# Kernel optimization log

Measured on AMD Instinct MI355X. Metric: run time of the kernel, lower is better.

Reference implementation:

```python
import jax, jax.numpy as jnp
import numpy as np

L = 2          # n layers
P = 768        # input_p_dim
Q = 768        # input_q_dim
H = 768        # hidden (nhids[i])
A = 768        # attention dim
B, T, TQ = 16, 128, 128
EPS = 1e-6


def setup_inputs() -> dict:
    key = jax.random.key(0)
    ks = jax.random.split(key, 12)
    stdv = 1.0 / np.sqrt(H)
    u = lambda k, shp: jax.random.uniform(k, shp, jnp.float32, -stdv, stdv)
    return {
        "input_p": jax.random.normal(ks[0], (B, T, P), jnp.float32),
        "mask_p": jnp.ones((B, T), jnp.float32),
        "input_q": jax.random.normal(ks[1], (B, TQ, Q), jnp.float32),
        "mask_q": jnp.ones((B, TQ), jnp.float32),
        # LSTMCell params (stacked over layers; input size = in_d + Q = P + Q)
        "W_ih": u(ks[2], (L, P + Q, 4 * H)),
        "W_hh": u(ks[3], (L, H, 4 * H)),
        "bias": jnp.zeros((L, 4 * H), jnp.float32),
        # LayerNorm params (gamma=1, beta=0 as in reset_parameters-style init)
        "ln_i_gamma": jnp.ones((L, 4 * H), jnp.float32),
        "ln_i_beta": jnp.zeros((L, 4 * H), jnp.float32),
        "ln_h_gamma": jnp.ones((L, 4 * H), jnp.float32),
        "ln_h_beta": jnp.zeros((L, 4 * H), jnp.float32),
        "ln_c_gamma": jnp.ones((L, H), jnp.float32),
        "ln_c_beta": jnp.zeros((L, H), jnp.float32),
        # match-attention params
        "Wq": u(ks[4], (L, Q, A)),
        "Wp": u(ks[5], (L, P, A)),   # in_d == P == H for both layers
        "Wr": u(ks[6], (L, H, A)),
        "w_att": u(ks[7], (L, A)),
        "b_att": u(ks[8], (L, A)),
    }


def _layernorm(x, gamma, beta, mask):
    # Faithful to the repo's LayerNorm: mean over last dim, var over dim=1
    # (identical for 2D x), unbiased variance (torch default), eps added twice.
    mean = x.mean(-1, keepdims=True)
    var = x.var(-1, ddof=1, keepdims=True)
    out = gamma * (x - mean) / (jnp.sqrt(var + EPS) + EPS) + beta
    return out * mask[:, None]


def reference(input_p, mask_p, input_q, mask_q, W_ih, W_hh, bias,
              ln_i_gamma, ln_i_beta, ln_h_gamma, ln_h_beta,
              ln_c_gamma, ln_c_beta, Wq, Wp, Wr, w_att, b_att):
    nlayers, hid = W_hh.shape[0], W_hh.shape[1]
    bsz, tlen, _ = input_p.shape
    # q @ Wq is time-invariant: hoist out of the recurrence. (L, B, Tq, A)
    qWq = jnp.einsum("bsd,lda->lbsa", input_q, Wq)

    def step(carry, xs):
        h, c = carry                      # each (L, B, H)
        p_t, m_t = xs                     # (B, P), (B,)
        m = m_t[:, None]
        cur = p_t
        hs, cs = [], []
        for d in range(nlayers):
            # --- match attention over q, conditioned on (cur, h_tm1) ---
            s = cur @ Wp[d] + h[d] @ Wr[d] + b_att[d]          # (B, A)
            G = jnp.tanh(qWq[d] + s[:, None, :])               # (B, Tq, A)
            scores = G @ w_att[d]                              # (B, Tq)
            scores = jnp.where(mask_q > 0, scores, -1e9)
            alpha = jax.nn.softmax(scores, axis=-1)
            weighted = jnp.einsum("bs,bsd->bd", alpha, input_q)
            x = jnp.concatenate([cur, weighted], axis=-1)      # (B, in_d + Q)
            # --- LSTM cell with inline layernorm + masking ---
            wi = _layernorm(x @ W_ih[d], ln_i_gamma[d], ln_i_beta[d], m_t)
            wh = _layernorm(h[d] @ W_hh[d], ln_h_gamma[d], ln_h_beta[d], m_t)
            pre = wi + wh + bias[d]
            f, i, o, g = jnp.split(pre, 4, axis=-1)            # order: f,i,o,g
            c1 = jax.nn.sigmoid(f) * c[d] + jax.nn.sigmoid(i) * jnp.tanh(g)
            c1 = c1 * m + c[d] * (1.0 - m)
            h1 = jax.nn.sigmoid(o) * jnp.tanh(
                _layernorm(c1, ln_c_gamma[d], ln_c_beta[d], m_t))
            h1 = h1 * m + h[d] * (1.0 - m)
            hs.append(h1)
            cs.append(c1)
            cur = h1
        return (jnp.stack(hs), jnp.stack(cs)), cur             # emit top-layer h

    h0 = jnp.zeros((nlayers, bsz, hid), input_p.dtype)
    c0 = jnp.zeros_like(h0)
    xs = (jnp.transpose(input_p, (1, 0, 2)), jnp.transpose(mask_p, (1, 0)))
    _, ys = jax.lax.scan(step, (h0, c0), xs)                   # ys: (T, B, H)
    states = jnp.transpose(ys, (1, 0, 2))                      # (B, T, H)
    return (states, mask_p)
```

## Files before the change

kernel.cpp:

```cpp
#include <hip/hip_runtime.h>
#include <math.h>

#define NBLK 512
#define NTHR 256

typedef float f32x4 __attribute__((ext_vector_type(4)));

__device__ __forceinline__ float2 ld2a(const float* p){
    unsigned long long u = __hip_atomic_load((const unsigned long long*)p,
                                             __ATOMIC_RELAXED, __HIP_MEMORY_SCOPE_AGENT);
    float2 r;
    r.x = __uint_as_float((unsigned)u);
    r.y = __uint_as_float((unsigned)(u >> 32));
    return r;
}
__device__ __forceinline__ void st2a(float* p, float a, float b){
    unsigned long long u = (unsigned long long)__float_as_uint(a)
                         | ((unsigned long long)__float_as_uint(b) << 32);
    __hip_atomic_store((unsigned long long*)p, u,
                       __ATOMIC_RELAXED, __HIP_MEMORY_SCOPE_AGENT);
}
__device__ __forceinline__ float ld1a(const float* p){
    unsigned u = __hip_atomic_load((const unsigned*)p, __ATOMIC_RELAXED, __HIP_MEMORY_SCOPE_AGENT);
    return __uint_as_float(u);
}
__device__ __forceinline__ void st1a(float* p, float v){
    __hip_atomic_store((unsigned*)p, __float_as_uint(v), __ATOMIC_RELAXED, __HIP_MEMORY_SCOPE_AGENT);
}

__device__ __forceinline__ float fsigmoid(float x){ return 1.0f/(1.0f + __expf(-x)); }
__device__ __forceinline__ float ftanh(float x){
    float e = __expf(2.0f*x);
    return 1.0f - 2.0f/(e + 1.0f);
}
__device__ __forceinline__ float dot4(f32x4 a, f32x4 b){
    return a.x*b.x + a.y*b.y + a.z*b.z + a.w*b.w;
}

struct Params {
    const float* input_p; const float* mask_p; const float* input_q; const float* mask_q;
    const float* W_ih; const float* W_hh; const float* bias;
    const float* ln_i_g; const float* ln_i_b; const float* ln_h_g; const float* ln_h_b;
    const float* ln_c_g; const float* ln_c_b;
    const float* Wq; const float* Wp; const float* Wr; const float* w_att; const float* b_att;
    float* out;
    float* qWq;
    float* iqT;
    float* pWp0;
    float* pWih0;
    float* h;
    float* c;
    float* sP;
    float* whP;
    float* cwP;
    float* wiP;
    float* wghtd;
    float* escore;
    unsigned* bar;
};

__device__ __forceinline__ void gsync(unsigned* bar, int bid, unsigned n){
    __syncthreads();
    if (threadIdx.x == 0){
        unsigned* leaf = bar + 128 + (bid >> 4)*32;
        unsigned old = __hip_atomic_fetch_add(leaf, 1u, __ATOMIC_RELAXED, __HIP_MEMORY_SCOPE_AGENT);
        if ((old & 15u) == 15u){
            unsigned rold = __hip_atomic_fetch_add(bar + 32, 1u, __ATOMIC_RELAXED, __HIP_MEMORY_SCOPE_AGENT);
            if ((rold & 31u) == 31u){
                __hip_atomic_store(bar, n + 1u, __ATOMIC_RELEASE, __HIP_MEMORY_SCOPE_AGENT);
            }
        }
        int spins = 0;
        while (__hip_atomic_load(bar, __ATOMIC_RELAXED, __HIP_MEMORY_SCOPE_AGENT) < n + 1u){
            __builtin_amdgcn_s_sleep(4);
            if (++spins > 1024){
                (void)__hip_atomic_load(bar, __ATOMIC_ACQUIRE, __HIP_MEMORY_SCOPE_AGENT);
                spins = 0;
            }
        }
    }
    __syncthreads();
}

__device__ __forceinline__ void stageA(
    const float* Aptr, int ars, int aco, int k0, bool coh, float* Ash, int tid)
{
    #pragma unroll
    for (int rep = 0; rep < 6; rep++){
        int i2 = tid + rep*256;
        int r = i2 / 96, kk = (i2 % 96)*2;
        const float* src = Aptr + (size_t)r*ars + aco + k0 + kk;
        float2 v;
        if (coh) v = ld2a(src); else v = *(const float2*)src;
        Ash[r*192 + kk]     = v.x;
        Ash[r*192 + kk + 1] = v.y;
    }
    __syncthreads();
}

__device__ __forceinline__ void mm192f(
    const float* W, int N, float* outP, int cbase, int k0,
    const float* Ash, int tid)
{
    int cg = tid & 15, rg = tid >> 4;
    int col = cbase + cg*4;
    const float* Wc = W + (size_t)k0*N + col;
    const float* Arow = Ash + rg*192;
    f32x4 acc = {0,0,0,0};
    f32x4 wA[8], wB[8];
    #pragma unroll
    for (int j = 0; j < 8; j++) wA[j] = *(const f32x4*)(Wc + (size_t)j*N);
    for (int kb = 0; kb < 192; kb += 16){
        #pragma unroll
        for (int j = 0; j < 8; j++) wB[j] = *(const f32x4*)(Wc + (size_t)(kb+8+j)*N);
        #pragma unroll
        for (int j = 0; j < 8; j++) acc += Arow[kb+j]*wA[j];
        if (kb < 176){
            #pragma unroll
            for (int j = 0; j < 8; j++) wA[j] = *(const f32x4*)(Wc + (size_t)(kb+16+j)*N);
        }
        #pragma unroll
        for (int j = 0; j < 8; j++) acc += Arow[kb+8+j]*wB[j];
    }
    float* o = outP + (size_t)rg*N + col;
    st2a(o,   acc.x, acc.y);
    st2a(o+2, acc.z, acc.w);
}

__device__ __forceinline__ float bsum4(float v, float* red, int tid){
    #pragma unroll
    for (int off = 32; off; off >>= 1) v += __shfl_xor(v, off);
    __syncthreads();
    if ((tid & 63) == 0) red[tid >> 6] = v;
    __syncthreads();
    float s = red[0]+red[1]+red[2]+red[3];
    __syncthreads();
    return s;
}

__global__ __launch_bounds__(NTHR, 2) void coop_kernel(Params p)
{
    __shared__ float smem[6936];
    const int tid = threadIdx.x;
    const int bid = blockIdx.x;
    unsigned n = 0;

    {
        int gid = bid*NTHR + tid;
        if (gid < 24576) st2a(p.h + gid*2, 0.f, 0.f);
        if (gid < 2048)  p.out[(size_t)16*128*768 + gid] = p.mask_p[gid];
    }
    gsync(p.bar, bid, n); n++;

    for (int t = 0; t < 128; ++t){
        for (int d = 0; d < 2; ++d){
            const float* h_d = p.h + (size_t)d*12288;

            {
                int ntile = (d == 0) ? 60 : 120;
                if (bid < ntile*4){
                    int tile = bid >> 2, kc = bid & 3, k0 = kc*192;
                    if (d == 0){
                        stageA(h_d, 768, 0, k0, true, smem, tid);
                        if (tile < 12){
                            mm192f(p.Wr, 768, p.sP + (size_t)kc*12288, tile*64, k0, smem, tid);
                        } else {
                            mm192f(p.W_hh, 3072, p.whP + (size_t)kc*49152, (tile-12)*64, k0, smem, tid);
                        }
                    } else {
                        bool useCur = (tile >= 12 && tile < 24) || (tile >= 72);
                        stageA(useCur ? p.h : h_d, 768, 0, k0, true, smem, tid);
                        if (tile < 12){
                            mm192f(p.Wr + (size_t)589824, 768,
                                   p.sP + (size_t)kc*12288, tile*64, k0, smem, tid);
                        } else if (tile < 24){
                            mm192f(p.Wp + (size_t)589824, 768,
                                   p.sP + (size_t)(4+kc)*12288, (tile-12)*64, k0, smem, tid);
                        } else if (tile < 72){
                            mm192f(p.W_hh + (size_t)2359296, 3072,
                                   p.whP + (size_t)kc*49152, (tile-24)*64, k0, smem, tid);
                        } else {
                            mm192f(p.W_ih + (size_t)4718592, 3072,
                                   p.cwP + (size_t)kc*49152, (tile-72)*64, k0, smem, tid);
                        }
                    }
                }
            }
            gsync(p.bar, bid, n); n++;

            if (bid < 256){
                int b = bid >> 4, sq0 = (bid & 15)*8;
                float* s_sh  = smem;
                float* wa_sh = smem + 768;
                if (tid < 192){
                    f32x4 acc = *(const f32x4*)(p.b_att + d*768 + tid*4);
                    if (d == 0){
                        f32x4 pv = *(const f32x4*)(p.pWp0 + ((size_t)b*128 + t)*768 + tid*4);
                        acc += pv;
                    }
                    int ncp = (d == 0) ? 4 : 8;
                    for (int cp = 0; cp < ncp; cp++){
                        const float* src = p.sP + (size_t)cp*12288 + b*768 + tid*4;
                        float2 u0 = ld2a(src);
                        float2 u1 = ld2a(src + 2);
                        acc.x += u0.x; acc.y += u0.y; acc.z += u1.x; acc.w += u1.y;
                    }
                    *(f32x4*)&s_sh[tid*4] = acc;
                } else {
                    int i0 = tid - 192;
                    for (int r = 0; r < 3; r++){
                        int i = i0 + r*64;
                        *(f32x4*)&wa_sh[i*4] = *(const f32x4*)(p.w_att + d*768 + i*4);
                    }
                }
                __syncthreads();
                int sq = sq0 + (tid >> 5), l = tid & 31;
                const float* qrow = p.qWq + ((size_t)(d*2048 + b*128 + sq))*768;
                float part = 0.f;
                #pragma unroll
                for (int i = 0; i < 6; i++){
                    int a = i*128 + l*4;
                    f32x4 q  = *(const f32x4*)(qrow + a);
                    f32x4 s4 = *(const f32x4*)(s_sh + a);
                    f32x4 w4 = *(const f32x4*)(wa_sh + a);
                    part += ftanh(q.x + s4.x)*w4.x + ftanh(q.y + s4.y)*w4.y
                          + ftanh(q.z + s4.z)*w4.z + ftanh(q.w + s4.w)*w4.w;
                }
                #pragma unroll
                for (int off = 16; off; off >>= 1) part += __shfl_xor(part, off, 32);
                if (l == 0){
                    float e = (p.mask_q[b*128 + sq] > 0.f) ? __expf(part) : 0.f;
                    st1a(p.escore + b*128 + sq, e);
                }
            }
            gsync(p.bar, bid, n); n++;

            if (bid < 64){
                int b = bid >> 2, cg = bid & 3;
                float* e_sh = smem;
                if (tid < 128) e_sh[tid] = ld1a(p.escore + b*128 + tid);
                __syncthreads();
                if (tid < 64){
                    float v = e_sh[tid] + e_sh[tid + 64];
                    #pragma unroll
                    for (int off = 32; off; off >>= 1) v += __shfl_xor(v, off);
                    if (tid == 0) e_sh[128] = 1.0f / v;
                }
                __syncthreads();
                float inv = e_sh[128];
                if (tid < 192){
                    int cc = cg*192 + tid;
                    const float* ip = p.iqT + ((size_t)b*768 + cc)*128;
                    float acc = 0.f;
                    #pragma unroll 8
                    for (int j = 0; j < 32; j++){
                        f32x4 q  = *(const f32x4*)(ip + j*4);
                        f32x4 e4 = *(const f32x4*)&e_sh[j*4];
                        acc += dot4(q, e4);
                    }
                    st1a(p.wghtd + b*768 + cc, acc*inv);
                }
            }
            gsync(p.bar, bid, n); n++;

            if (bid < 192){
                int tile = bid >> 2, kc = bid & 3, k0 = kc*192;
                stageA(p.wghtd, 768, 0, k0, true, smem, tid);
                mm192f(p.W_ih + (size_t)d*4718592 + (size_t)768*3072, 3072,
                       p.wiP + (size_t)kc*49152, tile*64, k0, smem, tid);
            }
            gsync(p.bar, bid, n); n++;

            if (bid < 16){
                const int b = bid;
                float* wi_sh = smem;
                float* wh_sh = smem + 3072;
                float* c_sh  = smem + 6144;
                float* red   = smem + 6928;
                const float mm = p.mask_p[b*128 + t];
                const float* gi = p.ln_i_g + d*3072; const float* bi = p.ln_i_b + d*3072;
                const float* gh = p.ln_h_g + d*3072; const float* bh = p.ln_h_b + d*3072;
                const float* gc = p.ln_c_g + d*768;  const float* bc = p.ln_c_b + d*768;
                const float* bias_d = p.bias + d*3072;

                float swi=0,qwi=0,swh=0,qwh=0;
                #pragma unroll
                for (int rep = 0; rep < 3; rep++){
                    int j4 = tid + rep*256;
                    int base = b*3072 + j4*4;
                    f32x4 a = {0,0,0,0};
                    f32x4 hvec = {0,0,0,0};
                    #pragma unroll
                    for (int cp = 0; cp < 4; cp++){
                        const float* s0 = p.wiP + (size_t)cp*49152 + base;
                        float2 u0 = ld2a(s0);
                        float2 u1 = ld2a(s0 + 2);
                        a.x += u0.x; a.y += u0.y; a.z += u1.x; a.w += u1.y;
                        const float* s1 = p.whP + (size_t)cp*49152 + base;
                        float2 v0 = ld2a(s1);
                        float2 v1 = ld2a(s1 + 2);
                        hvec.x += v0.x; hvec.y += v0.y; hvec.z += v1.x; hvec.w += v1.y;
                    }
                    if (d == 0){
                        f32x4 pv = *(const f32x4*)(p.pWih0 + ((size_t)b*128 + t)*3072 + j4*4);
                        a += pv;
                    } else {
                        #pragma unroll
                        for (int cp = 0; cp < 4; cp++){
                            const float* s2 = p.cwP + (size_t)cp*49152 + base;
                            float2 w0 = ld2a(s2);
                            float2 w1 = ld2a(s2 + 2);
                            a.x += w0.x; a.y += w0.y; a.z += w1.x; a.w += w1.y;
                        }
                    }
                    *(f32x4*)&wi_sh[j4*4] = a;
                    *(f32x4*)&wh_sh[j4*4] = hvec;
                    swi += a.x+a.y+a.z+a.w;
                    qwi += dot4(a,a);
                    swh += hvec.x+hvec.y+hvec.z+hvec.w;
                    qwh += dot4(hvec,hvec);
                }
                swi = bsum4(swi, red, tid);
                qwi = bsum4(qwi, red, tid);
                swh = bsum4(swh, red, tid);
                qwh = bsum4(qwh, red, tid);
                float mi = swi/3072.f, vi = fmaxf((qwi - 3072.f*mi*mi)/3071.f, 0.f);
                float mh = swh/3072.f, vh = fmaxf((qwh - 3072.f*mh*mh)/3071.f, 0.f);
                float ivi = 1.f/(sqrtf(vi + 1e-6f) + 1e-6f);
                float ivh = 1.f/(sqrtf(vh + 1e-6f) + 1e-6f);

                for (int j = tid; j < 3072; j += NTHR){
                    float pre = mm*(gi[j]*(wi_sh[j]-mi)*ivi + bi[j])
                              + mm*(gh[j]*(wh_sh[j]-mh)*ivh + bh[j])
                              + bias_d[j];
                    wi_sh[j] = pre;
                }
                __syncthreads();

                float sc=0,qc=0;
                for (int idx = tid; idx < 384; idx += NTHR){
                    int u = idx*2;
                    float2 c_old = ld2a(p.c + (size_t)d*12288 + b*768 + u);
                    float f0  = wi_sh[u],        f1  = wi_sh[u+1];
                    float i0  = wi_sh[768+u],    i1  = wi_sh[768+u+1];
                    float g0  = wi_sh[2304+u],   g1  = wi_sh[2304+u+1];
                    float c10 = fsigmoid(f0)*c_old.x + fsigmoid(i0)*ftanh(g0);
                    float c11 = fsigmoid(f1)*c_old.y + fsigmoid(i1)*ftanh(g1);
                    c10 = c10*mm + c_old.x*(1.f - mm);
                    c11 = c11*mm + c_old.y*(1.f - mm);
                    st2a(p.c + (size_t)d*12288 + b*768 + u, c10, c11);
                    c_sh[u] = c10; c_sh[u+1] = c11;
                    sc += c10 + c11; qc += c10*c10 + c11*c11;
                }
                sc = bsum4(sc, red, tid);
                qc = bsum4(qc, red, tid);
                float mc = sc/768.f, vc = fmaxf((qc - 768.f*mc*mc)/767.f, 0.f);
                float ivc = 1.f/(sqrtf(vc + 1e-6f) + 1e-6f);

                for (int idx = tid; idx < 384; idx += NTHR){
                    int u = idx*2;
                    float2 h_old = ld2a(p.h + (size_t)d*12288 + b*768 + u);
                    float o0 = wi_sh[1536+u], o1 = wi_sh[1536+u+1];
                    float l0 = (gc[u]*(c_sh[u]-mc)*ivc + bc[u])*mm;
                    float l1 = (gc[u+1]*(c_sh[u+1]-mc)*ivc + bc[u+1])*mm;
                    float h10 = fsigmoid(o0)*ftanh(l0);
                    float h11 = fsigmoid(o1)*ftanh(l1);
                    h10 = h10*mm + h_old.x*(1.f - mm);
                    h11 = h11*mm + h_old.y*(1.f - mm);
                    st2a(p.h + (size_t)d*12288 + b*768 + u, h10, h11);
                    if (d == 1){
                        float2 ov = { h10, h11 };
                        *(float2*)(p.out + ((size_t)b*128 + t)*768 + u) = ov;
                    }
                }
            }
            gsync(p.bar, bid, n); n++;
        }
    }
}

__global__ __launch_bounds__(256) void k_mm_pre(
    const float* __restrict__ Ain, const float* __restrict__ W,
    float* __restrict__ C, int ldw, int ncols)
{
    __shared__ float Ash[16][772];
    int rowbase = blockIdx.y*16;
    for (int r = 0; r < 16; r++)
        for (int i = threadIdx.x; i < 768; i += 256)
            Ash[r][i] = Ain[(size_t)(rowbase + r)*768 + i];
    __syncthreads();
    int lane = threadIdx.x & 63;
    int colq = lane & 15, rsub = lane >> 4, wq = threadIdx.x >> 6;
    int r = wq*4 + rsub;
    int col = blockIdx.x*64 + colq*4;
    float4 acc = {0.f,0.f,0.f,0.f};
    const float* Wc = W + col;
    for (int k = 0; k < 768; k += 4){
        float4 a4 = *(const float4*)&Ash[r][k];
        float4 w0 = *(const float4*)(Wc + (size_t)(k+0)*ldw);
        float4 w1 = *(const float4*)(Wc + (size_t)(k+1)*ldw);
        float4 w2 = *(const float4*)(Wc + (size_t)(k+2)*ldw);
        float4 w3 = *(const float4*)(Wc + (size_t)(k+3)*ldw);
        acc.x += a4.x*w0.x + a4.y*w1.x + a4.z*w2.x + a4.w*w3.x;
        acc.y += a4.x*w0.y + a4.y*w1.y + a4.z*w2.y + a4.w*w3.y;
        acc.z += a4.x*w0.z + a4.y*w1.z + a4.z*w2.z + a4.w*w3.z;
        acc.w += a4.x*w0.w + a4.y*w1.w + a4.z*w2.w + a4.w*w3.w;
    }
    *(float4*)(C + (size_t)(rowbase + r)*ncols + col) = acc;
}

__global__ __launch_bounds__(256) void k_transq(
    const float* __restrict__ iq, float* __restrict__ iqT)
{
    __shared__ float Tsh[32][136];
    int c0 = blockIdx.x*32, b = blockIdx.y;
    for (int rep = 0; rep < 4; rep++){
        int idx = threadIdx.x + rep*256;
        int sq = idx >> 3, cq = idx & 7;
        float4 v = *(const float4*)(iq + ((size_t)b*128 + sq)*768 + c0 + cq*4);
        Tsh[cq*4+0][sq] = v.x;
        Tsh[cq*4+1][sq] = v.y;
        Tsh[cq*4+2][sq] = v.z;
        Tsh[cq*4+3][sq] = v.w;
    }
    __syncthreads();
    for (int rep = 0; rep < 4; rep++){
        int idx = threadIdx.x + rep*256;
        int cl = idx >> 5, sq4 = (idx & 31)*4;
        float4 v = *(const float4*)&Tsh[cl][sq4];
        *(float4*)(iqT + ((size_t)b*768 + c0 + cl)*128 + sq4) = v;
    }
}

extern "C" void kernel_launch(void* const* d_in, const int* in_sizes, int n_in,
                              void* d_out, int out_size, void* d_ws, size_t ws_size,
                              hipStream_t stream)
{
    (void)in_sizes; (void)n_in; (void)out_size; (void)ws_size;
    Params P;
    P.input_p = (const float*)d_in[0];
    P.mask_p  = (const float*)d_in[1];
    P.input_q = (const float*)d_in[2];
    P.mask_q  = (const float*)d_in[3];
    P.W_ih    = (const float*)d_in[4];
    P.W_hh    = (const float*)d_in[5];
    P.bias    = (const float*)d_in[6];
    P.ln_i_g  = (const float*)d_in[7];
    P.ln_i_b  = (const float*)d_in[8];
    P.ln_h_g  = (const float*)d_in[9];
    P.ln_h_b  = (const float*)d_in[10];
    P.ln_c_g  = (const float*)d_in[11];
    P.ln_c_b  = (const float*)d_in[12];
    P.Wq      = (const float*)d_in[13];
    P.Wp      = (const float*)d_in[14];
    P.Wr      = (const float*)d_in[15];
    P.w_att   = (const float*)d_in[16];
    P.b_att   = (const float*)d_in[17];
    P.out     = (float*)d_out;

    float* ws = (float*)d_ws;
    size_t off = 0;
    auto alloc = [&](size_t nfloat)->float*{
        float* r = ws + off;
        off += (nfloat + 63) & ~(size_t)63;
        return r;
    };
    P.qWq    = alloc((size_t)2*2048*768);
    P.iqT    = alloc((size_t)16*768*128);
    P.pWp0   = alloc((size_t)2048*768);
    P.pWih0  = alloc((size_t)2048*3072);
    P.h      = alloc(24576);
    P.c      = alloc(24576);
    P.sP     = alloc((size_t)8*16*768);
    P.whP    = alloc((size_t)4*16*3072);
    P.cwP    = alloc((size_t)4*16*3072);
    P.wiP    = alloc((size_t)4*16*3072);
    P.wghtd  = alloc(12288);
    P.escore = alloc(2048);
    P.bar    = (unsigned*)alloc(2048);

    hipMemsetAsync((void*)P.bar, 0, 2048*sizeof(unsigned), stream);
    k_mm_pre<<<dim3(12,128), 256, 0, stream>>>(P.input_q, P.Wq, P.qWq, 768, 768);
    k_mm_pre<<<dim3(12,128), 256, 0, stream>>>(P.input_q, P.Wq + (size_t)589824,
                                               P.qWq + (size_t)2048*768, 768, 768);
    k_mm_pre<<<dim3(12,128), 256, 0, stream>>>(P.input_p, P.Wp, P.pWp0, 768, 768);
    k_mm_pre<<<dim3(48,128), 256, 0, stream>>>(P.input_p, P.W_ih, P.pWih0, 3072, 3072);
    k_transq<<<dim3(24,16), 256, 0, stream>>>(P.input_q, P.iqT);
    coop_kernel<<<dim3(NBLK), dim3(NTHR), 0, stream>>>(P);
}
```

Measured before the change: 18.70 ms.

## Reschedule recurrent phases to overlap layer work and split K into eight chunks

```diff
diff --git a/kernel.cpp b/kernel.cpp
--- a/kernel.cpp
+++ b/kernel.cpp
@@ -5,6 +5,17 @@
 #define NTHR 256
 
 typedef float f32x4 __attribute__((ext_vector_type(4)));
+
+__device__ __forceinline__ f32x4 ld4c(const float* p){
+    f32x4 v;
+    asm volatile("global_load_dwordx4 %0, %1, off sc0 sc1" : "=v"(v) : "v"(p) : "memory");
+    return v;
+}
+__device__ __forceinline__ void st4c(float* p, f32x4 v){
+    asm volatile("global_store_dwordx4 %0, %1, off sc0 sc1" :: "v"(p), "v"(v) : "memory");
+}
+__device__ __forceinline__ void vm0(){ asm volatile("s_waitcnt vmcnt(0)" ::: "memory"); }
+__device__ __forceinline__ f32x4 ldr4(f32x4 v){ asm volatile("" : "+v"(v)); return v; }
 
 __device__ __forceinline__ float2 ld2a(const float* p){
     unsigned long long u = __hip_atomic_load((const unsigned long long*)p,
@@ -50,11 +61,20 @@
     float* pWih0;
     float* h;
     float* c;
-    float* sP;
-    float* whP;
-    float* cwP;
+    float* sP0;
+    float* whP0;
+    float* sP1h;
+    float* whP1;
+    float* sP1c;
+    float* cwP1;
     float* wiP;
-    float* wghtd;
+    float* whR0;
+    float* whR1;
+    float* cwR1;
+    float* sR0;
+    float* sR1h;
+    float* wghtd0;
+    float* wghtd1;
     float* escore;
     unsigned* bar;
 };
@@ -82,51 +102,6 @@
     __syncthreads();
 }
 
-__device__ __forceinline__ void stageA(
-    const float* Aptr, int ars, int aco, int k0, bool coh, float* Ash, int tid)
-{
-    #pragma unroll
-    for (int rep = 0; rep < 6; rep++){
-        int i2 = tid + rep*256;
-        int r = i2 / 96, kk = (i2 % 96)*2;
-        const float* src = Aptr + (size_t)r*ars + aco + k0 + kk;
-        float2 v;
-        if (coh) v = ld2a(src); else v = *(const float2*)src;
-        Ash[r*192 + kk]     = v.x;
-        Ash[r*192 + kk + 1] = v.y;
-    }
-    __syncthreads();
-}
-
-__device__ __forceinline__ void mm192f(
-    const float* W, int N, float* outP, int cbase, int k0,
-    const float* Ash, int tid)
-{
-    int cg = tid & 15, rg = tid >> 4;
-    int col = cbase + cg*4;
-    const float* Wc = W + (size_t)k0*N + col;
-    const float* Arow = Ash + rg*192;
-    f32x4 acc = {0,0,0,0};
-    f32x4 wA[8], wB[8];
-    #pragma unroll
-    for (int j = 0; j < 8; j++) wA[j] = *(const f32x4*)(Wc + (size_t)j*N);
-    for (int kb = 0; kb < 192; kb += 16){
-        #pragma unroll
-        for (int j = 0; j < 8; j++) wB[j] = *(const f32x4*)(Wc + (size_t)(kb+8+j)*N);
-        #pragma unroll
-        for (int j = 0; j < 8; j++) acc += Arow[kb+j]*wA[j];
-        if (kb < 176){
-            #pragma unroll
-            for (int j = 0; j < 8; j++) wA[j] = *(const f32x4*)(Wc + (size_t)(kb+16+j)*N);
-        }
-        #pragma unroll
-        for (int j = 0; j < 8; j++) acc += Arow[kb+8+j]*wB[j];
-    }
-    float* o = outP + (size_t)rg*N + col;
-    st2a(o,   acc.x, acc.y);
-    st2a(o+2, acc.z, acc.w);
-}
-
 __device__ __forceinline__ float bsum4(float v, float* red, int tid){
     #pragma unroll
     for (int off = 32; off; off >>= 1) v += __shfl_xor(v, off);
@@ -145,237 +120,328 @@
     const int bid = blockIdx.x;
     unsigned n = 0;
 
+    auto stage96 = [&](const float* src, int k0){
+        int r0 = tid/24, kk0 = (tid%24)*4;
+        f32x4 v0 = ld4c(src + (size_t)r0*768 + k0 + kk0);
+        f32x4 v1;
+        int i1 = tid + 256, r1 = i1/24, kk1 = (i1%24)*4;
+        if (tid < 128) v1 = ld4c(src + (size_t)r1*768 + k0 + kk1);
+        vm0();
+        v0 = ldr4(v0); *(f32x4*)&smem[r0*96 + kk0] = v0;
+        if (tid < 128){ v1 = ldr4(v1); *(f32x4*)&smem[r1*96 + kk1] = v1; }
+        __syncthreads();
+    };
+
+    auto mm96w = [&](const float* W, int N, float* outP, int cbase, int k0){
+        int cg = tid & 31, rg = tid >> 5;
+        int col = cbase + cg*4;
+        const float* Wc = W + (size_t)k0*N + col;
+        const float* A0 = smem + rg*96;
+        const float* A1 = smem + (rg+8)*96;
+        f32x4 acc0 = {0,0,0,0}, acc1 = {0,0,0,0};
+        for (int kb = 0; kb < 96; kb += 8){
+            f32x4 w[8];
+            #pragma unroll
+            for (int j = 0; j < 8; j++)
+                w[j] = *(const f32x4*)(Wc + (size_t)(kb+j)*N);
+            #pragma unroll
+            for (int j = 0; j < 8; j++){
+                acc0 += A0[kb+j]*w[j];
+                acc1 += A1[kb+j]*w[j];
+            }
+        }
+        float* o = outP + (size_t)rg*N + col;
+        st4c(o, acc0);
+        st4c(o + (size_t)8*N, acc1);
+        __syncthreads();
+    };
+
+    auto s2a = [&](int d, const float* sR, const float* sPc, float* esc){
+        int bb = (bid - 256) >> 4, sq0 = ((bid - 256) & 15)*8;
+        float* s_sh  = smem;
+        float* wa_sh = smem + 768;
+        if (tid < 192){
+            f32x4 acc;
+            f32x4 v0 = ld4c(sR + bb*768 + tid*4);
+            f32x4 vc[8];
+            if (sPc){
+                #pragma unroll
+                for (int cp = 0; cp < 8; cp++)
+                    vc[cp] = ld4c(sPc + (size_t)cp*12288 + bb*768 + tid*4);
+            }
+            vm0();
+            acc = ldr4(v0);
+            if (sPc){
+                #pragma unroll
+                for (int cp = 0; cp < 8; cp++){ vc[cp] = ldr4(vc[cp]); acc += vc[cp]; }
+            }
+            *(f32x4*)&s_sh[tid*4] = acc;
+        } else {
+            int i0 = tid - 192;
+            for (int rr = 0; rr < 3; rr++){
+                int i = i0 + rr*64;
+                *(f32x4*)&wa_sh[i*4] = *(const f32x4*)(p.w_att + d*768 + i*4);
+            }
+        }
+        __syncthreads();
+        int sq = sq0 + (tid >> 5), l = tid & 31;
+        const float* qrow = p.qWq + ((size_t)(d*2048 + bb*128 + sq))*768;
+        float part = 0.f;
+        #pragma unroll
+        for (int i = 0; i < 6; i++){
+            int a = i*128 + l*4;
+            f32x4 q  = *(const f32x4*)(qrow + a);
+            f32x4 s4 = *(const f32x4*)(s_sh + a);
+            f32x4 w4 = *(const f32x4*)(wa_sh + a);
+            part += ftanh(q.x + s4.x)*w4.x + ftanh(q.y + s4.y)*w4.y
+                  + ftanh(q.z + s4.z)*w4.z + ftanh(q.w + s4.w)*w4.w;
+        }
+        #pragma unroll
+        for (int off = 16; off; off >>= 1) part += __shfl_xor(part, off, 32);
+        if (l == 0){
+            float e = (p.mask_q[bb*128 + sq] > 0.f) ? __expf(part) : 0.f;
+            st1a(esc + bb*128 + sq, e);
+        }
+        __syncthreads();
+    };
+
+    auto s2b = [&](float* wout){
+        int bb = bid >> 2, cg = bid & 3;
+        float* e_sh = smem;
+        if (tid < 128) e_sh[tid] = ld1a(p.escore + bb*128 + tid);
+        __syncthreads();
+        if (tid < 64){
+            float v = e_sh[tid] + e_sh[tid + 64];
+            #pragma unroll
+            for (int off = 32; off; off >>= 1) v += __shfl_xor(v, off);
+            if (tid == 0) e_sh[128] = 1.0f / v;
+        }
+        __syncthreads();
+        float inv = e_sh[128];
+        if (tid < 192){
+            int cc = cg*192 + tid;
+            const float* ip = p.iqT + ((size_t)bb*768 + cc)*128;
+            float acc = 0.f;
+            #pragma unroll 8
+            for (int j = 0; j < 32; j++){
+                f32x4 q  = *(const f32x4*)(ip + j*4);
+                f32x4 e4 = *(const f32x4*)&e_sh[j*4];
+                acc += dot4(q, e4);
+            }
+            st1a(wout + bb*768 + cc, acc*inv);
+        }
+        __syncthreads();
+    };
+
+    auto red8big = [&](const float* src, float* dst, int boff){
+        int gid = (bid - boff)*NTHR + tid;
+        f32x4 v[8];
+        #pragma unroll
+        for (int cp = 0; cp < 8; cp++)
+            v[cp] = ld4c(src + (size_t)cp*49152 + gid*4);
+        vm0();
+        f32x4 a = {0,0,0,0};
+        #pragma unroll
+        for (int cp = 0; cp < 8; cp++){ v[cp] = ldr4(v[cp]); a += v[cp]; }
+        st4c(dst + gid*4, a);
+    };
+
+    auto redS = [&](const float* srcP, float* dst, int d, const float* pw, int tt, int boff){
+        int bb = bid - boff;
+        if (tid < 192){
+            f32x4 v[8];
+            #pragma unroll
+            for (int cp = 0; cp < 8; cp++)
+                v[cp] = ld4c(srcP + (size_t)cp*12288 + bb*768 + tid*4);
+            vm0();
+            f32x4 a = *(const f32x4*)(p.b_att + d*768 + tid*4);
+            if (pw) a += *(const f32x4*)(pw + ((size_t)bb*128 + tt)*768 + tid*4);
+            #pragma unroll
+            for (int cp = 0; cp < 8; cp++){ v[cp] = ldr4(v[cp]); a += v[cp]; }
+            st4c(dst + bb*768 + tid*4, a);
+        }
+    };
+
+    auto gates = [&](int d, int t){
+        int bb = bid;
+        float* wi_sh = smem;
+        float* wh_sh = smem + 3072;
+        float* c_sh  = smem + 6144;
+        float* red   = smem + 6928;
+        const float mmv = p.mask_p[bb*128 + t];
+        const float* gi = p.ln_i_g + d*3072; const float* bi = p.ln_i_b + d*3072;
+        const float* gh = p.ln_h_g + d*3072; const float* bh = p.ln_h_b + d*3072;
+        const float* gc = p.ln_c_g + d*768;  const float* bc = p.ln_c_b + d*768;
+        const float* bias_d = p.bias + d*3072;
+        const float* whR = d ? p.whR1 : p.whR0;
+
+        float swi=0,qwi=0,swh=0,qwh=0;
+        #pragma unroll
+        for (int rep = 0; rep < 3; rep++){
+            int j4 = tid + rep*256;
+            int base = bb*3072 + j4*4;
+            f32x4 v[8], wv, cv;
+            #pragma unroll
+            for (int cp = 0; cp < 8; cp++)
+                v[cp] = ld4c(p.wiP + (size_t)cp*49152 + base);
+            wv = ld4c(whR + base);
+            if (d == 1) cv = ld4c(p.cwR1 + base);
+            vm0();
+            f32x4 a = {0,0,0,0};
+            #pragma unroll
+            for (int cp = 0; cp < 8; cp++){ v[cp] = ldr4(v[cp]); a += v[cp]; }
+            if (d == 0){
+                a += *(const f32x4*)(p.pWih0 + ((size_t)bb*128 + t)*3072 + j4*4);
+            } else {
+                cv = ldr4(cv); a += cv;
+            }
+            wv = ldr4(wv);
+            *(f32x4*)&wi_sh[j4*4] = a;
+            *(f32x4*)&wh_sh[j4*4] = wv;
+            swi += a.x+a.y+a.z+a.w;   qwi += dot4(a,a);
+            swh += wv.x+wv.y+wv.z+wv.w; qwh += dot4(wv,wv);
+        }
+        swi = bsum4(swi, red, tid);
+        qwi = bsum4(qwi, red, tid);
+        swh = bsum4(swh, red, tid);
+        qwh = bsum4(qwh, red, tid);
+        float mi = swi/3072.f, vi = fmaxf((qwi - 3072.f*mi*mi)/3071.f, 0.f);
+        float mh = swh/3072.f, vh = fmaxf((qwh - 3072.f*mh*mh)/3071.f, 0.f);
+        float ivi = 1.f/(sqrtf(vi + 1e-6f) + 1e-6f);
+        float ivh = 1.f/(sqrtf(vh + 1e-6f) + 1e-6f);
+
+        for (int j = tid; j < 3072; j += NTHR){
+            float pre = mmv*(gi[j]*(wi_sh[j]-mi)*ivi + bi[j])
+                      + mmv*(gh[j]*(wh_sh[j]-mh)*ivh + bh[j])
+                      + bias_d[j];
+            wi_sh[j] = pre;
+        }
+        __syncthreads();
+
+        float sc=0,qc=0;
+        for (int idx = tid; idx < 384; idx += NTHR){
+            int u = idx*2;
+            float2 c_old = ld2a(p.c + (size_t)d*12288 + bb*768 + u);
+            float f0  = wi_sh[u],        f1  = wi_sh[u+1];
+            float i0  = wi_sh[768+u],    i1  = wi_sh[768+u+1];
+            float g0  = wi_sh[2304+u],   g1  = wi_sh[2304+u+1];
+            float c10 = fsigmoid(f0)*c_old.x + fsigmoid(i0)*ftanh(g0);
+            float c11 = fsigmoid(f1)*c_old.y + fsigmoid(i1)*ftanh(g1);
+            c10 = c10*mmv + c_old.x*(1.f - mmv);
+            c11 = c11*mmv + c_old.y*(1.f - mmv);
+            st2a(p.c + (size_t)d*12288 + bb*768 + u, c10, c11);
+            c_sh[u] = c10; c_sh[u+1] = c11;
+            sc += c10 + c11; qc += c10*c10 + c11*c11;
+        }
+        sc = bsum4(sc, red, tid);
+        qc = bsum4(qc, red, tid);
+        float mc = sc/768.f, vc = fmaxf((qc - 768.f*mc*mc)/767.f, 0.f);
+        float ivc = 1.f/(sqrtf(vc + 1e-6f) + 1e-6f);
+
+        for (int idx = tid; idx < 384; idx += NTHR){
+            int u = idx*2;
+            float2 h_old = ld2a(p.h + (size_t)d*12288 + bb*768 + u);
+            float o0 = wi_sh[1536+u], o1 = wi_sh[1536+u+1];
+            float l0 = (gc[u]*(c_sh[u]-mc)*ivc + bc[u])*mmv;
+            float l1 = (gc[u+1]*(c_sh[u+1]-mc)*ivc + bc[u+1])*mmv;
+            float h10 = fsigmoid(o0)*ftanh(l0);
+            float h11 = fsigmoid(o1)*ftanh(l1);
+            h10 = h10*mmv + h_old.x*(1.f - mmv);
+            h11 = h11*mmv + h_old.y*(1.f - mmv);
+            st2a(p.h + (size_t)d*12288 + bb*768 + u, h10, h11);
+            if (d == 1){
+                float2 ov = { h10, h11 };
+                *(float2*)(p.out + ((size_t)bb*128 + t)*768 + u) = ov;
+            }
+        }
+        __syncthreads();
+    };
+
     {
         int gid = bid*NTHR + tid;
-        if (gid < 24576) st2a(p.h + gid*2, 0.f, 0.f);
-        if (gid < 2048)  p.out[(size_t)16*128*768 + gid] = p.mask_p[gid];
+        f32x4 z = {0,0,0,0};
+        for (int i4 = gid; i4 < 135168; i4 += NBLK*NTHR)
+            st4c(p.h + (size_t)i4*4, z);
+        if (gid < 2048) p.out[(size_t)16*128*768 + gid] = p.mask_p[gid];
     }
     gsync(p.bar, bid, n); n++;
 
+    if (bid >= 16 && bid < 64)      red8big(p.whP0, p.whR0, 16);
+    else if (bid >= 64 && bid < 80) redS(p.sP0, p.sR0, 0, p.pWp0, 0, 64);
+    gsync(p.bar, bid, n); n++;
+
     for (int t = 0; t < 128; ++t){
-        for (int d = 0; d < 2; ++d){
-            const float* h_d = p.h + (size_t)d*12288;
-
-            {
-                int ntile = (d == 0) ? 60 : 120;
-                if (bid < ntile*4){
-                    int tile = bid >> 2, kc = bid & 3, k0 = kc*192;
-                    if (d == 0){
-                        stageA(h_d, 768, 0, k0, true, smem, tid);
-                        if (tile < 12){
-                            mm192f(p.Wr, 768, p.sP + (size_t)kc*12288, tile*64, k0, smem, tid);
-                        } else {
-                            mm192f(p.W_hh, 3072, p.whP + (size_t)kc*49152, (tile-12)*64, k0, smem, tid);
-                        }
-                    } else {
-                        bool useCur = (tile >= 12 && tile < 24) || (tile >= 72);
-                        stageA(useCur ? p.h : h_d, 768, 0, k0, true, smem, tid);
-                        if (tile < 12){
-                            mm192f(p.Wr + (size_t)589824, 768,
-                                   p.sP + (size_t)kc*12288, tile*64, k0, smem, tid);
-                        } else if (tile < 24){
-                            mm192f(p.Wp + (size_t)589824, 768,
-                                   p.sP + (size_t)(4+kc)*12288, (tile-12)*64, k0, smem, tid);
-                        } else if (tile < 72){
-                            mm192f(p.W_hh + (size_t)2359296, 3072,
-                                   p.whP + (size_t)kc*49152, (tile-24)*64, k0, smem, tid);
-                        } else {
-                            mm192f(p.W_ih + (size_t)4718592, 3072,
-                                   p.cwP + (size_t)kc*49152, (tile-72)*64, k0, smem, tid);
-                        }
-                    }
-                }
-            }
-            gsync(p.bar, bid, n); n++;
-
-            if (bid < 256){
-                int b = bid >> 4, sq0 = (bid & 15)*8;
-                float* s_sh  = smem;
-                float* wa_sh = smem + 768;
-                if (tid < 192){
-                    f32x4 acc = *(const f32x4*)(p.b_att + d*768 + tid*4);
-                    if (d == 0){
-                        f32x4 pv = *(const f32x4*)(p.pWp0 + ((size_t)b*128 + t)*768 + tid*4);
-                        acc += pv;
-                    }
-                    int ncp = (d == 0) ? 4 : 8;
-                    for (int cp = 0; cp < ncp; cp++){
-                        const float* src = p.sP + (size_t)cp*12288 + b*768 + tid*4;
-                        float2 u0 = ld2a(src);
-                        float2 u1 = ld2a(src + 2);
-                        acc.x += u0.x; acc.y += u0.y; acc.z += u1.x; acc.w += u1.y;
-                    }
-                    *(f32x4*)&s_sh[tid*4] = acc;
-                } else {
-                    int i0 = tid - 192;
-                    for (int r = 0; r < 3; r++){
-                        int i = i0 + r*64;
-                        *(f32x4*)&wa_sh[i*4] = *(const f32x4*)(p.w_att + d*768 + i*4);
-                    }
-                }
-                __syncthreads();
-                int sq = sq0 + (tid >> 5), l = tid & 31;
-                const float* qrow = p.qWq + ((size_t)(d*2048 + b*128 + sq))*768;
-                float part = 0.f;
-                #pragma unroll
-                for (int i = 0; i < 6; i++){
-                    int a = i*128 + l*4;
-                    f32x4 q  = *(const f32x4*)(qrow + a);
-                    f32x4 s4 = *(const f32x4*)(s_sh + a);
-                    f32x4 w4 = *(const f32x4*)(wa_sh + a);
-                    part += ftanh(q.x + s4.x)*w4.x + ftanh(q.y + s4.y)*w4.y
-                          + ftanh(q.z + s4.z)*w4.z + ftanh(q.w + s4.w)*w4.w;
-                }
-                #pragma unroll
-                for (int off = 16; off; off >>= 1) part += __shfl_xor(part, off, 32);
-                if (l == 0){
-                    float e = (p.mask_q[b*128 + sq] > 0.f) ? __expf(part) : 0.f;
-                    st1a(p.escore + b*128 + sq, e);
-                }
-            }
-            gsync(p.bar, bid, n); n++;
-
-            if (bid < 64){
-                int b = bid >> 2, cg = bid & 3;
-                float* e_sh = smem;
-                if (tid < 128) e_sh[tid] = ld1a(p.escore + b*128 + tid);
-                __syncthreads();
-                if (tid < 64){
-                    float v = e_sh[tid] + e_sh[tid + 64];
-                    #pragma unroll
-                    for (int off = 32; off; off >>= 1) v += __shfl_xor(v, off);
-                    if (tid == 0) e_sh[128] = 1.0f / v;
-                }
-                __syncthreads();
-                float inv = e_sh[128];
-                if (tid < 192){
-                    int cc = cg*192 + tid;
-                    const float* ip = p.iqT + ((size_t)b*768 + cc)*128;
-                    float acc = 0.f;
-                    #pragma unroll 8
-                    for (int j = 0; j < 32; j++){
-                        f32x4 q  = *(const f32x4*)(ip + j*4);
-                        f32x4 e4 = *(const f32x4*)&e_sh[j*4];
-                        acc += dot4(q, e4);
-                    }
-                    st1a(p.wghtd + b*768 + cc, acc*inv);
-                }
-            }
-            gsync(p.bar, bid, n); n++;
-
-            if (bid < 192){
-                int tile = bid >> 2, kc = bid & 3, k0 = kc*192;
-                stageA(p.wghtd, 768, 0, k0, true, smem, tid);
-                mm192f(p.W_ih + (size_t)d*4718592 + (size_t)768*3072, 3072,
-                       p.wiP + (size_t)kc*49152, tile*64, k0, smem, tid);
-            }
-            gsync(p.bar, bid, n); n++;
-
-            if (bid < 16){
-                const int b = bid;
-                float* wi_sh = smem;
-                float* wh_sh = smem + 3072;
-                float* c_sh  = smem + 6144;
-                float* red   = smem + 6928;
-                const float mm = p.mask_p[b*128 + t];
-                const float* gi = p.ln_i_g + d*3072; const float* bi = p.ln_i_b + d*3072;
-                const float* gh = p.ln_h_g + d*3072; const float* bh = p.ln_h_b + d*3072;
-                const float* gc = p.ln_c_g + d*768;  const float* bc = p.ln_c_b + d*768;
-                const float* bias_d = p.bias + d*3072;
-
-                float swi=0,qwi=0,swh=0,qwh=0;
-                #pragma unroll
-                for (int rep = 0; rep < 3; rep++){
-                    int j4 = tid + rep*256;
-                    int base = b*3072 + j4*4;
-                    f32x4 a = {0,0,0,0};
-                    f32x4 hvec = {0,0,0,0};
-                    #pragma unroll
-                    for (int cp = 0; cp < 4; cp++){
-                        const float* s0 = p.wiP + (size_t)cp*49152 + base;
-                        float2 u0 = ld2a(s0);
-                        float2 u1 = ld2a(s0 + 2);
-                        a.x += u0.x; a.y += u0.y; a.z += u1.x; a.w += u1.y;
-                        const float* s1 = p.whP + (size_t)cp*49152 + base;
-                        float2 v0 = ld2a(s1);
-                        float2 v1 = ld2a(s1 + 2);
-                        hvec.x += v0.x; hvec.y += v0.y; hvec.z += v1.x; hvec.w += v1.y;
-                    }
-                    if (d == 0){
-                        f32x4 pv = *(const f32x4*)(p.pWih0 + ((size_t)b*128 + t)*3072 + j4*4);
-                        a += pv;
-                    } else {
-                        #pragma unroll
-                        for (int cp = 0; cp < 4; cp++){
-                            const float* s2 = p.cwP + (size_t)cp*49152 + base;
-                            float2 w0 = ld2a(s2);
-                            float2 w1 = ld2a(s2 + 2);
-                            a.x += w0.x; a.y += w0.y; a.z += w1.x; a.w += w1.y;
-                        }
-                    }
-                    *(f32x4*)&wi_sh[j4*4] = a;
-                    *(f32x4*)&wh_sh[j4*4] = hvec;
-                    swi += a.x+a.y+a.z+a.w;
-                    qwi += dot4(a,a);
-                    swh += hvec.x+hvec.y+hvec.z+hvec.w;
-                    qwh += dot4(hvec,hvec);
-                }
-                swi = bsum4(swi, red, tid);
-                qwi = bsum4(qwi, red, tid);
-                swh = bsum4(swh, red, tid);
-                qwh = bsum4(qwh, red, tid);
-                float mi = swi/3072.f, vi = fmaxf((qwi - 3072.f*mi*mi)/3071.f, 0.f);
-                float mh = swh/3072.f, vh = fmaxf((qwh - 3072.f*mh*mh)/3071.f, 0.f);
-                float ivi = 1.f/(sqrtf(vi + 1e-6f) + 1e-6f);
-                float ivh = 1.f/(sqrtf(vh + 1e-6f) + 1e-6f);
-
-                for (int j = tid; j < 3072; j += NTHR){
-                    float pre = mm*(gi[j]*(wi_sh[j]-mi)*ivi + bi[j])
-                              + mm*(gh[j]*(wh_sh[j]-mh)*ivh + bh[j])
-                              + bias_d[j];
-                    wi_sh[j] = pre;
-                }
-                __syncthreads();
-
-                float sc=0,qc=0;
-                for (int idx = tid; idx < 384; idx += NTHR){
-                    int u = idx*2;
-                    float2 c_old = ld2a(p.c + (size_t)d*12288 + b*768 + u);
-                    float f0  = wi_sh[u],        f1  = wi_sh[u+1];
-                    float i0  = wi_sh[768+u],    i1  = wi_sh[768+u+1];
-                    float g0  = wi_sh[2304+u],   g1  = wi_sh[2304+u+1];
-                    float c10 = fsigmoid(f0)*c_old.x + fsigmoid(i0)*ftanh(g0);
-                    float c11 = fsigmoid(f1)*c_old.y + fsigmoid(i1)*ftanh(g1);
-                    c10 = c10*mm + c_old.x*(1.f - mm);
-                    c11 = c11*mm + c_old.y*(1.f - mm);
-                    st2a(p.c + (size_t)d*12288 + b*768 + u, c10, c11);
-                    c_sh[u] = c10; c_sh[u+1] = c11;
-                    sc += c10 + c11; qc += c10*c10 + c11*c11;
-                }
-                sc = bsum4(sc, red, tid);
-                qc = bsum4(qc, red, tid);
-                float mc = sc/768.f, vc = fmaxf((qc - 768.f*mc*mc)/767.f, 0.f);
-                float ivc = 1.f/(sqrtf(vc + 1e-6f) + 1e-6f);
-
-                for (int idx = tid; idx < 384; idx += NTHR){
-                    int u = idx*2;
-                    float2 h_old = ld2a(p.h + (size_t)d*12288 + b*768 + u);
-                    float o0 = wi_sh[1536+u], o1 = wi_sh[1536+u+1];
-                    float l0 = (gc[u]*(c_sh[u]-mc)*ivc + bc[u])*mm;
-                    float l1 = (gc[u+1]*(c_sh[u+1]-mc)*ivc + bc[u+1])*mm;
-                    float h10 = fsigmoid(o0)*ftanh(l0);
-                    float h11 = fsigmoid(o1)*ftanh(l1);
-                    h10 = h10*mm + h_old.x*(1.f - mm);
-                    h11 = h11*mm + h_old.y*(1.f - mm);
-                    st2a(p.h + (size_t)d*12288 + b*768 + u, h10, h11);
-                    if (d == 1){
-                        float2 ov = { h10, h11 };
-                        *(float2*)(p.out + ((size_t)b*128 + t)*768 + u) = ov;
-                    }
-                }
-            }
-            gsync(p.bar, bid, n); n++;
-        }
+        if (bid < 240){
+            int tile = bid >> 3, kc = bid & 7, k0 = kc*96;
+            stage96(p.h + 12288, k0);
+            if (tile < 6)
+                mm96w(p.Wr + (size_t)589824, 768, p.sP1h + (size_t)kc*12288, tile*128, k0);
+            else
+                mm96w(p.W_hh + (size_t)2359296, 3072, p.whP1 + (size_t)kc*49152, (tile-6)*128, k0);
+        } else if (bid >= 256){
+            s2a(0, p.sR0, nullptr, p.escore);
+        }
+        gsync(p.bar, bid, n); n++;
+
+        if (bid < 64)                    s2b(p.wghtd0);
+        else if (bid >= 64 && bid < 112) red8big(p.whP1, p.whR1, 64);
+        gsync(p.bar, bid, n); n++;
+
+        if (bid < 192){
+            int tile = bid >> 3, kc = bid & 7, k0 = kc*96;
+            stage96(p.wghtd0, k0);
+            mm96w(p.W_ih + (size_t)2359296, 3072, p.wiP + (size_t)kc*49152, tile*128, k0);
+        }
+        gsync(p.bar, bid, n); n++;
+
+        if (bid < 16) gates(0, t);
+        gsync(p.bar, bid, n); n++;
+
+        if (bid < 240){
+            int tile = bid >> 3, kc = bid & 7, k0 = kc*96;
+            stage96(p.h, k0);
+            if (tile < 6)
+                mm96w(p.Wp + (size_t)589824, 768, p.sP1c + (size_t)kc*12288, tile*128, k0);
+            else
+                mm96w(p.W_ih + (size_t)4718592, 3072, p.cwP1 + (size_t)kc*49152, (tile-6)*128, k0);
+        } else if (bid >= 240 && bid < 256){
+            redS(p.sP1h, p.sR1h, 1, nullptr, 0, 240);
+        }
+        gsync(p.bar, bid, n); n++;
+
+        if (bid < 240){
+            int tile = bid >> 3, kc = bid & 7, k0 = kc*96;
+            stage96(p.h, k0);
+            if (tile < 6)
+                mm96w(p.Wr, 768, p.sP0 + (size_t)kc*12288, tile*128, k0);
+            else
+                mm96w(p.W_hh, 3072, p.whP0 + (size_t)kc*49152, (tile-6)*128, k0);
+        } else if (bid >= 256){
+            s2a(1, p.sR1h, p.sP1c, p.escore);
+        }
+        gsync(p.bar, bid, n); n++;
+
+        if (bid < 64)                    s2b(p.wghtd1);
+        else if (bid >= 64 && bid < 112) red8big(p.cwP1, p.cwR1, 64);
+        gsync(p.bar, bid, n); n++;
+
+        if (bid < 192){
+            int tile = bid >> 3, kc = bid & 7, k0 = kc*96;
+            stage96(p.wghtd1, k0);
+            mm96w(p.W_ih + (size_t)4718592 + (size_t)2359296, 3072,
+                  p.wiP + (size_t)kc*49152, tile*128, k0);
+        }
+        gsync(p.bar, bid, n); n++;
+
+        if (bid < 16){
+            gates(1, t);
+        } else if (bid >= 16 && bid < 64){
+            red8big(p.whP0, p.whR0, 16);
+        } else if (bid >= 64 && bid < 80){
+            int tt = (t + 1 < 128) ? t + 1 : 127;
+            redS(p.sP0, p.sR0, 0, p.pWp0, tt, 64);
+        }
+        gsync(p.bar, bid, n); n++;
     }
 }
 
@@ -471,15 +537,24 @@
     P.pWih0  = alloc((size_t)2048*3072);
     P.h      = alloc(24576);
     P.c      = alloc(24576);
-    P.sP     = alloc((size_t)8*16*768);
-    P.whP    = alloc((size_t)4*16*3072);
-    P.cwP    = alloc((size_t)4*16*3072);
-    P.wiP    = alloc((size_t)4*16*3072);
-    P.wghtd  = alloc(12288);
+    P.sP0    = alloc((size_t)8*12288);
+    P.whP0   = alloc((size_t)8*49152);
+    P.sP1h   = alloc((size_t)8*12288);
+    P.whP1   = alloc((size_t)8*49152);
+    P.sP1c   = alloc((size_t)8*12288);
+    P.cwP1   = alloc((size_t)8*49152);
+    P.wiP    = alloc((size_t)8*49152);
+    P.whR0   = alloc(49152);
+    P.whR1   = alloc(49152);
+    P.cwR1   = alloc(49152);
+    P.sR0    = alloc(12288);
+    P.sR1h   = alloc(12288);
+    P.wghtd0 = alloc(12288);
+    P.wghtd1 = alloc(12288);
     P.escore = alloc(2048);
     P.bar    = (unsigned*)alloc(2048);
 
-    hipMemsetAsync((void*)P.bar, 0, 2048*sizeof(unsigned), stream);
+    (void)hipMemsetAsync((void*)P.bar, 0, 2048*sizeof(unsigned), stream);
     k_mm_pre<<<dim3(12,128), 256, 0, stream>>>(P.input_q, P.Wq, P.qWq, 768, 768);
     k_mm_pre<<<dim3(12,128), 256, 0, stream>>>(P.input_q, P.Wq + (size_t)589824,
                                                P.qWq + (size_t)2048*768, 768, 768);
```

Result: slower. 30.96 ms (+65.6%).
